# Optimization experiments

Hardware: AMD Instinct MI355X
Metric: run time of the kernel (lower is better)

## Reference

```python
import jax, jax.numpy as jnp
import numpy as np

NUM_EXPERTS = 8
HIDDEN = 2048
EXPERT_DIM = 2048  # intermediate_size per shard (tp_size=1)
TOTAL_TOKENS = 32768  # divisible by NUM_EXPERTS


def setup_inputs() -> dict:
    key = jax.random.key(0)
    k1, k2, k3 = jax.random.split(key, 3)
    hidden_states = jax.random.normal(k1, (TOTAL_TOKENS, HIDDEN), dtype=jnp.float32)
    # (E, H, 2*D): gate and up projections concatenated on last dim
    gate_up_proj = jax.random.normal(k2, (NUM_EXPERTS, HIDDEN, 2 * EXPERT_DIM), dtype=jnp.float32) * 0.02
    # (E, D, H)
    down_proj = jax.random.normal(k3, (NUM_EXPERTS, EXPERT_DIM, HIDDEN), dtype=jnp.float32) * 0.02
    return {"hidden_states": hidden_states, "gate_up_proj": gate_up_proj, "down_proj": down_proj}


def reference(hidden_states, gate_up_proj, down_proj):
    E, H = gate_up_proj.shape[0], gate_up_proj.shape[1]
    # tokens are pre-sorted per expert: (E, T, H)
    x = hidden_states.reshape(E, -1, H)
    # grouped GEMM: (E,T,H) @ (E,H,2D) -> (E,T,2D)
    gate_up = jnp.einsum('eth,ehd->etd', x, gate_up_proj)
    gate, up = jnp.split(gate_up, 2, axis=-1)
    # SwiGLU epilogue then down projection: (E,T,D) @ (E,D,H) -> (E,T,H)
    act = up * jax.nn.silu(gate)
    out = jnp.einsum('etd,edh->eth', act, down_proj)
    # tp_size=1 -> all_reduce is identity
    return out.reshape(-1, H)
```

## Files before the change

### kernel.cpp

```cpp
#include <hip/hip_runtime.h>


#define E_EXPERTS 8
#define HID 2048
#define TPE 4096

typedef __bf16 bf16_t;
typedef __bf16 bf16x4 __attribute__((ext_vector_type(4)));
typedef __bf16 bf16x8 __attribute__((ext_vector_type(8)));
typedef float f32x4 __attribute__((ext_vector_type(4)));

#define GLOAD16(src, dst)                                               \
  __builtin_amdgcn_global_load_lds(                                     \
      (const __attribute__((address_space(1))) void*)(src),             \
      (__attribute__((address_space(3))) void*)(dst), 16, 0, 0)

__global__ void cvt_f32_bf16_kernel(const float* __restrict__ in,
                                    bf16_t* __restrict__ out, long n4) {
  long i = (long)blockIdx.x * blockDim.x + threadIdx.x;
  const long stride = (long)gridDim.x * blockDim.x;
  const float4* in4 = (const float4*)in;
  bf16x4* out4 = (bf16x4*)out;
  for (; i < n4; i += stride) {
    float4 v = in4[i];
    bf16x4 o = {(bf16_t)v.x, (bf16_t)v.y, (bf16_t)v.z, (bf16_t)v.w};
    out4[i] = o;
  }
}

__global__ void transpose_cvt_kernel(const float* __restrict__ W,
                                     bf16_t* __restrict__ WT, int K, int N) {
  __shared__ float tile[64][65];
  const int e = blockIdx.z;
  const float* Wp = W + (size_t)e * K * N;
  bf16_t* Tp = WT + (size_t)e * N * K;
  const int n0 = blockIdx.x * 64, k0 = blockIdx.y * 64;
  const int rr = threadIdx.x >> 4;
  const int cc = (threadIdx.x & 15) * 4;
#pragma unroll
  for (int p = 0; p < 4; ++p) {
    const int k = rr + p * 16;
    float4 v = *(const float4*)(Wp + (size_t)(k0 + k) * N + n0 + cc);
    tile[k][cc + 0] = v.x;
    tile[k][cc + 1] = v.y;
    tile[k][cc + 2] = v.z;
    tile[k][cc + 3] = v.w;
  }
  __syncthreads();
#pragma unroll
  for (int p = 0; p < 4; ++p) {
    const int n = rr + p * 16;
    bf16x4 o;
#pragma unroll
    for (int j = 0; j < 4; ++j) o[j] = (bf16_t)tile[cc + j][n];
    *(bf16x4*)(Tp + (size_t)(n0 + n) * K + k0 + cc) = o;
  }
}

template <bool FUSED>
__global__ __launch_bounds__(256, 2) void moe_gemm_kernel(
    const bf16_t* __restrict__ A, const bf16_t* __restrict__ B,
    void* __restrict__ Cout) {
  constexpr int BM = 128, BN = 128, BK = 32, K = 2048;
  constexpr int BROWS = FUSED ? 256 : 128;
  constexpr int NT = K / BK;
  constexpr size_t A_EXP = (size_t)TPE * K;
  constexpr size_t B_EXP = (size_t)(FUSED ? 4096 : 2048) * K;

  __shared__ alignas(16) bf16_t As[2][BM][BK];
  __shared__ alignas(16) bf16_t Bs[2][BROWS][BK];

  const int e = blockIdx.z;
  const int n0 = blockIdx.x * BN;
  const int t0 = blockIdx.y * BM;
  const int tid = threadIdx.x;
  const int wid = tid >> 6, lane = tid & 63;
  const int wr = wid >> 1, wc = wid & 1;

  const bf16_t* Ae = A + (size_t)e * A_EXP + (size_t)t0 * K;
  const bf16_t* Be = B + (size_t)e * B_EXP;

  const int lr = lane >> 2;
  const int lc = (lane & 3) * 8;

  f32x4 accg[4][4] = {};
  f32x4 accu[4][4] = {};

  auto stage = [&](int kt, int nb) {
    const int k0 = kt * BK;
#pragma unroll
    for (int jj = 0; jj < 2; ++jj) {
      const int j = wid * 2 + jj;
      GLOAD16(Ae + (size_t)(j * 16 + lr) * K + (k0 + lc), &As[nb][j * 16][0]);
    }
    if constexpr (FUSED) {
#pragma unroll
      for (int jj = 0; jj < 4; ++jj) {
        const int j = wid * 4 + jj;
        const int srow = (j >> 3) * 2048 + n0 + (j & 7) * 16 + lr;
        GLOAD16(Be + (size_t)srow * K + (k0 + lc), &Bs[nb][j * 16][0]);
      }
    } else {
#pragma unroll
      for (int jj = 0; jj < 2; ++jj) {
        const int j = wid * 2 + jj;
        GLOAD16(Be + (size_t)(n0 + j * 16 + lr) * K + (k0 + lc),
                &Bs[nb][j * 16][0]);
      }
    }
  };

  const int la = lane & 15, kg = (lane >> 4) * 8;

  auto compute = [&](int cb) {
    bf16x8 af[4], bg[4], bu[4];
#pragma unroll
    for (int m = 0; m < 4; ++m)
      af[m] = *(const bf16x8*)&As[cb][wr * 64 + m * 16 + la][kg];
#pragma unroll
    for (int n = 0; n < 4; ++n)
      bg[n] = *(const bf16x8*)&Bs[cb][wc * 64 + n * 16 + la][kg];
    if constexpr (FUSED) {
#pragma unroll
      for (int n = 0; n < 4; ++n)
        bu[n] = *(const bf16x8*)&Bs[cb][128 + wc * 64 + n * 16 + la][kg];
    }
#pragma unroll
    for (int m = 0; m < 4; ++m) {
#pragma unroll
      for (int n = 0; n < 4; ++n) {
        accg[m][n] = __builtin_amdgcn_mfma_f32_16x16x32_bf16(af[m], bg[n],
                                                             accg[m][n], 0, 0, 0);
        if constexpr (FUSED)
          accu[m][n] = __builtin_amdgcn_mfma_f32_16x16x32_bf16(
              af[m], bu[n], accu[m][n], 0, 0, 0);
      }
    }
  };

  stage(0, 0);
  __syncthreads();
  for (int kt = 0; kt < NT; ++kt) {
    if (kt + 1 < NT) stage(kt + 1, (kt + 1) & 1);
    compute(kt & 1);
    __syncthreads();
  }

  const int lg = lane >> 4;
  if constexpr (FUSED) {
    bf16_t* Cp = (bf16_t*)Cout + (size_t)e * A_EXP;
#pragma unroll
    for (int m = 0; m < 4; ++m)
#pragma unroll
      for (int n = 0; n < 4; ++n)
#pragma unroll
        for (int r = 0; r < 4; ++r) {
          const int row = t0 + wr * 64 + m * 16 + lg * 4 + r;
          const int col = n0 + wc * 64 + n * 16 + la;
          const float g = accg[m][n][r], u = accu[m][n][r];
          const float sv = 1.0f / (1.0f + __expf(-g));
          Cp[(size_t)row * 2048 + col] = (bf16_t)(u * g * sv);
        }
  } else {
    float* Cp = (float*)Cout + (size_t)e * A_EXP;
#pragma unroll
    for (int m = 0; m < 4; ++m)
#pragma unroll
      for (int n = 0; n < 4; ++n)
#pragma unroll
        for (int r = 0; r < 4; ++r) {
          const int row = t0 + wr * 64 + m * 16 + lg * 4 + r;
          const int col = n0 + wc * 64 + n * 16 + la;
          Cp[(size_t)row * 2048 + col] = accg[m][n][r];
        }
  }
}

extern "C" void kernel_launch(void* const* d_in, const int* in_sizes, int n_in,
                              void* d_out, int out_size, void* d_ws,
                              size_t ws_size, hipStream_t stream) {
  const float* hs = (const float*)d_in[0];
  const float* w1 = (const float*)d_in[1];
  const float* w2 = (const float*)d_in[2];

  char* ws = (char*)d_ws;
  bf16_t* xb = (bf16_t*)(ws);
  bf16_t* w1t = (bf16_t*)(ws + (size_t)134217728);
  bf16_t* w2t = (bf16_t*)(ws + (size_t)268435456);
  bf16_t* act = (bf16_t*)(ws + (size_t)335544320);

  const long n4 = (long)E_EXPERTS * TPE * HID / 4;
  cvt_f32_bf16_kernel<<<2048, 256, 0, stream>>>(hs, xb, n4);
  transpose_cvt_kernel<<<dim3(64, 32, 8), 256, 0, stream>>>(w1, w1t, 2048, 4096);
  transpose_cvt_kernel<<<dim3(32, 32, 8), 256, 0, stream>>>(w2, w2t, 2048, 2048);
  moe_gemm_kernel<true><<<dim3(16, 32, 8), 256, 0, stream>>>(xb, w1t, (void*)act);
  moe_gemm_kernel<false><<<dim3(16, 32, 8), 256, 0, stream>>>(act, w2t, d_out);
}
```

Baseline: 1.288 ms.

## Rewrite grouped GEMM as 256x256 8-wave ping-pong kernel with swizzled LDS

Replaces the 128x128 BK=32 GEMM with a 512-thread 256x256 BK=64 kernel. It splits each K tile into four MFMA quadrants interleaved with LDS reads and global-to-LDS prefetches, using explicit barriers, waitcnt and s_setprio. The LDS layout is XOR-swizzled to avoid bank conflicts, and gate/up rows are interleaved in 16-row groups so one accumulator tile holds both. Workgroup IDs are remapped across XCDs. The aim is to raise MFMA utilisation and data reuse, at the cost of heavy register pressure, 128KB of LDS, and fragile hand-tuned synchronisation.

Result: faster. 1.165 ms (-9.6%).

```diff
diff --git a/kernel.cpp b/kernel.cpp
--- a/kernel.cpp
+++ b/kernel.cpp
@@ -2,8 +2,8 @@
 
 
 #define E_EXPERTS 8
-#define HID 2048
 #define TPE 4096
+#define KD 2048
 
 typedef __bf16 bf16_t;
 typedef __bf16 bf16x4 __attribute__((ext_vector_type(4)));
@@ -57,123 +57,179 @@
   }
 }
 
-template <bool FUSED>
-__global__ __launch_bounds__(256, 2) void moe_gemm_kernel(
-    const bf16_t* __restrict__ A, const bf16_t* __restrict__ B,
+#define MMA_QUAD(QM, QN, BF)                                                 \
+  do {                                                                       \
+    _Pragma("unroll") for (int kk = 0; kk < 2; ++kk) {                       \
+      _Pragma("unroll") for (int m = 0; m < 4; ++m) {                        \
+        _Pragma("unroll") for (int n = 0; n < 2; ++n) {                      \
+          acc[(QM)*4 + m][(QN)*2 + n] =                                      \
+              __builtin_amdgcn_mfma_f32_16x16x32_bf16(                       \
+                  af[m][kk], BF[n][kk], acc[(QM)*4 + m][(QN)*2 + n], 0, 0, 0); \
+        }                                                                    \
+      }                                                                      \
+    }                                                                        \
+  } while (0)
+
+template <bool FUSED, int NTN>
+__global__ __launch_bounds__(512, 2) void moe_gemm8_kernel(
+    const bf16_t* __restrict__ A, const bf16_t* __restrict__ Bm,
     void* __restrict__ Cout) {
-  constexpr int BM = 128, BN = 128, BK = 32, K = 2048;
-  constexpr int BROWS = FUSED ? 256 : 128;
-  constexpr int NT = K / BK;
-  constexpr size_t A_EXP = (size_t)TPE * K;
-  constexpr size_t B_EXP = (size_t)(FUSED ? 4096 : 2048) * K;
-
-  __shared__ alignas(16) bf16_t As[2][BM][BK];
-  __shared__ alignas(16) bf16_t Bs[2][BROWS][BK];
-
-  const int e = blockIdx.z;
-  const int n0 = blockIdx.x * BN;
-  const int t0 = blockIdx.y * BM;
+  constexpr int NT = KD / 64;
+  constexpr int NWG = E_EXPERTS * 16 * NTN;
+
+  __shared__ alignas(16) bf16_t As[2][256][64];
+  __shared__ alignas(16) bf16_t Bs[2][256][64];
+
+  int wg = blockIdx.x;
+  wg = (wg & 7) * (NWG / 8) + (wg >> 3);
+  const int e = wg / (16 * NTN);
+  const int rem = wg % (16 * NTN);
+  const int mt = rem / NTN, ntile = rem % NTN;
+  const int t0 = mt * 256, n0 = ntile * 256;
+
   const int tid = threadIdx.x;
   const int wid = tid >> 6, lane = tid & 63;
-  const int wr = wid >> 1, wc = wid & 1;
-
-  const bf16_t* Ae = A + (size_t)e * A_EXP + (size_t)t0 * K;
-  const bf16_t* Be = B + (size_t)e * B_EXP;
-
-  const int lr = lane >> 2;
-  const int lc = (lane & 3) * 8;
-
-  f32x4 accg[4][4] = {};
-  f32x4 accu[4][4] = {};
-
-  auto stage = [&](int kt, int nb) {
-    const int k0 = kt * BK;
-#pragma unroll
-    for (int jj = 0; jj < 2; ++jj) {
-      const int j = wid * 2 + jj;
-      GLOAD16(Ae + (size_t)(j * 16 + lr) * K + (k0 + lc), &As[nb][j * 16][0]);
-    }
-    if constexpr (FUSED) {
-#pragma unroll
-      for (int jj = 0; jj < 4; ++jj) {
-        const int j = wid * 4 + jj;
-        const int srow = (j >> 3) * 2048 + n0 + (j & 7) * 16 + lr;
-        GLOAD16(Be + (size_t)srow * K + (k0 + lc), &Bs[nb][j * 16][0]);
+  const int wr = wid >> 2, wc = wid & 3;
+
+  const bf16_t* Ae = A + (size_t)e * TPE * KD + (size_t)t0 * KD;
+  const bf16_t* Be = Bm + (size_t)e * (size_t)(FUSED ? 4096 : 2048) * KD;
+
+  const int slr = lane >> 3;
+  const int sel = ((lane & 7) ^ slr) * 8;
+
+  auto stageA = [&](int kt, int h) {
+    const int ktw = (kt < NT) ? kt : kt - NT;
+    const int k0 = ktw * 64;
+    const int buf = kt & 1;
+#pragma unroll
+    for (int i = 0; i < 2; ++i) {
+      const int r0 = h * 128 + wid * 16 + i * 8;
+      GLOAD16(Ae + (size_t)(r0 + slr) * KD + k0 + sel, &As[buf][r0][0]);
+    }
+  };
+  auto stageB = [&](int kt, int h) {
+    const int ktw = (kt < NT) ? kt : kt - NT;
+    const int k0 = ktw * 64;
+    const int buf = kt & 1;
+#pragma unroll
+    for (int i = 0; i < 2; ++i) {
+      const int r0 = h * 128 + wid * 16 + i * 8;
+      const int R = n0 + r0 + slr;
+      int srow;
+      if constexpr (FUSED)
+        srow = ((R >> 5) << 4) + (R & 15) + ((R >> 4) & 1) * 2048;
+      else
+        srow = R;
+      GLOAD16(Be + (size_t)srow * KD + k0 + sel, &Bs[buf][r0][0]);
+    }
+  };
+
+  const int la = lane & 15, kg4 = lane >> 4;
+
+  f32x4 acc[8][4] = {};
+  bf16x8 af[4][2];
+  bf16x8 b0[2][2];
+  bf16x8 b1[2][2];
+
+  auto readA = [&](int buf, int qm) {
+#pragma unroll
+    for (int m = 0; m < 4; ++m) {
+      const int row = wr * 128 + qm * 64 + m * 16 + la;
+#pragma unroll
+      for (int kk = 0; kk < 2; ++kk) {
+        const int ch = ((kk * 4 + kg4) ^ (la & 7)) * 8;
+        af[m][kk] = *(const bf16x8*)&As[buf][row][ch];
       }
-    } else {
-#pragma unroll
-      for (int jj = 0; jj < 2; ++jj) {
-        const int j = wid * 2 + jj;
-        GLOAD16(Be + (size_t)(n0 + j * 16 + lr) * K + (k0 + lc),
-                &Bs[nb][j * 16][0]);
+    }
+  };
+  auto readB = [&](int buf, int qn, bf16x8 (&bf)[2][2]) {
+#pragma unroll
+    for (int n = 0; n < 2; ++n) {
+      const int row = wc * 64 + qn * 32 + n * 16 + la;
+#pragma unroll
+      for (int kk = 0; kk < 2; ++kk) {
+        const int ch = ((kk * 4 + kg4) ^ (la & 7)) * 8;
+        bf[n][kk] = *(const bf16x8*)&Bs[buf][row][ch];
       }
     }
   };
 
-  const int la = lane & 15, kg = (lane >> 4) * 8;
-
-  auto compute = [&](int cb) {
-    bf16x8 af[4], bg[4], bu[4];
-#pragma unroll
-    for (int m = 0; m < 4; ++m)
-      af[m] = *(const bf16x8*)&As[cb][wr * 64 + m * 16 + la][kg];
-#pragma unroll
-    for (int n = 0; n < 4; ++n)
-      bg[n] = *(const bf16x8*)&Bs[cb][wc * 64 + n * 16 + la][kg];
-    if constexpr (FUSED) {
-#pragma unroll
-      for (int n = 0; n < 4; ++n)
-        bu[n] = *(const bf16x8*)&Bs[cb][128 + wc * 64 + n * 16 + la][kg];
-    }
-#pragma unroll
-    for (int m = 0; m < 4; ++m) {
-#pragma unroll
-      for (int n = 0; n < 4; ++n) {
-        accg[m][n] = __builtin_amdgcn_mfma_f32_16x16x32_bf16(af[m], bg[n],
-                                                             accg[m][n], 0, 0, 0);
-        if constexpr (FUSED)
-          accu[m][n] = __builtin_amdgcn_mfma_f32_16x16x32_bf16(
-              af[m], bu[n], accu[m][n], 0, 0, 0);
-      }
-    }
-  };
-
-  stage(0, 0);
-  __syncthreads();
-  for (int kt = 0; kt < NT; ++kt) {
-    if (kt + 1 < NT) stage(kt + 1, (kt + 1) & 1);
-    compute(kt & 1);
-    __syncthreads();
+#define LGKM0 asm volatile("s_waitcnt lgkmcnt(0)" ::: "memory")
+#define VMC4 asm volatile("s_waitcnt vmcnt(4)" ::: "memory")
+#define BAR __builtin_amdgcn_s_barrier()
+#define PRIO1 __builtin_amdgcn_s_setprio(1)
+#define PRIO0 __builtin_amdgcn_s_setprio(0)
+
+  stageA(0, 0); stageA(0, 1);
+  stageB(0, 0); stageB(0, 1);
+  stageB(1, 0); stageB(1, 1);
+  VMC4;
+  BAR;
+
+  auto tile = [&](int kt, int buf) {
+    readA(buf, 0);
+    readB(buf, 0, b0);
+    stageA(kt + 1, 0);
+    BAR; LGKM0;
+    PRIO1; MMA_QUAD(0, 0, b0); PRIO0;
+    BAR;
+    readB(buf, 1, b1);
+    stageA(kt + 1, 1);
+    BAR; LGKM0;
+    PRIO1; MMA_QUAD(0, 1, b1); PRIO0;
+    BAR;
+    readA(buf, 1);
+    stageB(kt + 2, 0);
+    BAR; LGKM0;
+    PRIO1; MMA_QUAD(1, 1, b1); PRIO0;
+    BAR;
+    stageB(kt + 2, 1);
+    VMC4;
+    BAR;
+    PRIO1; MMA_QUAD(1, 0, b0); PRIO0;
+    BAR;
+  };
+
+  for (int kt = 0; kt < NT; kt += 2) {
+    tile(kt, 0);
+    tile(kt + 1, 1);
   }
 
   const int lg = lane >> 4;
+  const int rbase = t0 + wr * 128;
   if constexpr (FUSED) {
-    bf16_t* Cp = (bf16_t*)Cout + (size_t)e * A_EXP;
-#pragma unroll
-    for (int m = 0; m < 4; ++m)
-#pragma unroll
-      for (int n = 0; n < 4; ++n)
+    bf16_t* Cp = (bf16_t*)Cout + (size_t)e * TPE * KD;
+    const int jb = (n0 + wc * 64) >> 1;
+#pragma unroll
+    for (int m = 0; m < 8; ++m)
+#pragma unroll
+      for (int p = 0; p < 2; ++p)
 #pragma unroll
         for (int r = 0; r < 4; ++r) {
-          const int row = t0 + wr * 64 + m * 16 + lg * 4 + r;
-          const int col = n0 + wc * 64 + n * 16 + la;
-          const float g = accg[m][n][r], u = accu[m][n][r];
-          const float sv = 1.0f / (1.0f + __expf(-g));
-          Cp[(size_t)row * 2048 + col] = (bf16_t)(u * g * sv);
+          const int row = rbase + m * 16 + lg * 4 + r;
+          const int col = jb + p * 16 + la;
+          const float g = acc[m][2 * p][r], u = acc[m][2 * p + 1][r];
+          const float s = 1.0f / (1.0f + __expf(-g));
+          Cp[(size_t)row * KD + col] = (bf16_t)(u * g * s);
         }
   } else {
-    float* Cp = (float*)Cout + (size_t)e * A_EXP;
-#pragma unroll
-    for (int m = 0; m < 4; ++m)
+    float* Cp = (float*)Cout + (size_t)e * TPE * KD;
+#pragma unroll
+    for (int m = 0; m < 8; ++m)
 #pragma unroll
       for (int n = 0; n < 4; ++n)
 #pragma unroll
         for (int r = 0; r < 4; ++r) {
-          const int row = t0 + wr * 64 + m * 16 + lg * 4 + r;
+          const int row = rbase + m * 16 + lg * 4 + r;
           const int col = n0 + wc * 64 + n * 16 + la;
-          Cp[(size_t)row * 2048 + col] = accg[m][n][r];
+          Cp[(size_t)row * KD + col] = acc[m][n][r];
         }
   }
+#undef LGKM0
+#undef VMC4
+#undef BAR
+#undef PRIO1
+#undef PRIO0
 }
 
 extern "C" void kernel_launch(void* const* d_in, const int* in_sizes, int n_in,
@@ -189,10 +245,10 @@
   bf16_t* w2t = (bf16_t*)(ws + (size_t)268435456);
   bf16_t* act = (bf16_t*)(ws + (size_t)335544320);
 
-  const long n4 = (long)E_EXPERTS * TPE * HID / 4;
+  const long n4 = (long)E_EXPERTS * TPE * KD / 4;
   cvt_f32_bf16_kernel<<<2048, 256, 0, stream>>>(hs, xb, n4);
   transpose_cvt_kernel<<<dim3(64, 32, 8), 256, 0, stream>>>(w1, w1t, 2048, 4096);
   transpose_cvt_kernel<<<dim3(32, 32, 8), 256, 0, stream>>>(w2, w2t, 2048, 2048);
-  moe_gemm_kernel<true><<<dim3(16, 32, 8), 256, 0, stream>>>(xb, w1t, (void*)act);
-  moe_gemm_kernel<false><<<dim3(16, 32, 8), 256, 0, stream>>>(act, w2t, d_out);
-}
+  moe_gemm8_kernel<true, 16><<<2048, 512, 0, stream>>>(xb, w1t, (void*)act);
+  moe_gemm8_kernel<false, 8><<<1024, 512, 0, stream>>>(act, w2t, d_out);
+}
```
